# Performance work log

Measured on AMD Instinct MI355X. Metric: run time of the kernel, lower is better.

The kernel has to match this reference:

```python
import jax, jax.numpy as jnp
import numpy as np

B, N, C = 2, 20000, 256
TEST_MAX_BOX = 5000
IOU_THRESHOLDS = (0.4, 0.6, 0.8)
N_HIDDEN_LAYERS = 6  # six Conv1d(256,256,k=1)+LeakyReLU blocks in mask_w_layers


def setup_inputs() -> dict:
    key = jax.random.key(0)
    ks = jax.random.split(key, 8)
    # valid xyxy boxes: top-left in [0,900), w/h in [4,84)
    xy = jax.random.uniform(ks[0], (B, 2, N), dtype=jnp.float32) * 900.0
    wh = jax.random.uniform(ks[1], (B, 2, N), dtype=jnp.float32) * 80.0 + 4.0
    box = jnp.concatenate([xy, xy + wh], axis=1)              # [B,4,N]
    score = jax.random.uniform(ks[2], (B, 1, N), dtype=jnp.float32)
    feat = jax.random.normal(ks[3], (B, C, N), dtype=jnp.float32)
    W = jax.random.normal(ks[4], (N_HIDDEN_LAYERS, C, C), dtype=jnp.float32) * 0.02
    b = jnp.zeros((N_HIDDEN_LAYERS, C), dtype=jnp.float32)
    Wf = jax.random.normal(ks[5], (len(IOU_THRESHOLDS), C), dtype=jnp.float32) * 0.02
    bf = jnp.zeros((len(IOU_THRESHOLDS),), dtype=jnp.float32)
    return {"box": box, "score": score, "feat": feat, "W": W, "b": b, "Wf": Wf, "bf": bf}


def _box_iou(a, bxs):
    # a: [N,4], bxs: [M,4], xyxy -> [N,M] (torchvision ops.box_iou)
    area_a = (a[:, 2] - a[:, 0]) * (a[:, 3] - a[:, 1])
    area_b = (bxs[:, 2] - bxs[:, 0]) * (bxs[:, 3] - bxs[:, 1])
    lt = jnp.maximum(a[:, None, :2], bxs[None, :, :2])
    rb = jnp.minimum(a[:, None, 2:], bxs[None, :, 2:])
    wh = jnp.clip(rb - lt, 0.0)
    inter = wh[..., 0] * wh[..., 1]
    return inter / (area_a[:, None] + area_b[None, :] - inter)


def reference(box, score, feat, W, b, Wf, bf):
    # forward_test path of LMM
    boxT = jnp.swapaxes(box, 1, 2)                 # [B,N,4]
    s = jnp.swapaxes(score, 1, 2)[..., 0]          # [B,N]
    top_s, keep = jax.lax.top_k(s, TEST_MAX_BOX)   # [B,K] each, sorted desc
    boxK = jnp.take_along_axis(boxT, keep[..., None], axis=1)   # [B,K,4]
    featK = jnp.take_along_axis(feat, keep[:, None, :], axis=2)  # [B,C,K]

    iou = jax.vmap(_box_iou)(boxK, boxK)           # [B,K,K]
    idx = jnp.arange(TEST_MAX_BOX)
    masks = []
    for thr in IOU_THRESHOLDS:
        adjc = jnp.where(iou >= thr, 1.0, 0.0) * top_s[:, :, None]  # [B,K,K]
        max_idx = jnp.argmax(adjc, axis=1)                           # [B,K]
        masks.append((max_idx == idx[None, :]).astype(featK.dtype))
    masks = jnp.stack(masks, axis=1)               # [B,3,K]

    x = featK
    for l in range(N_HIDDEN_LAYERS):
        x = jax.nn.leaky_relu(jnp.einsum('oi,bik->bok', W[l], x) + b[l][:, None], 0.2)
    mask_w = jax.nn.softmax(jnp.einsum('oi,bik->bok', Wf, x) + bf[:, None], axis=1)  # [B,3,K]

    loc_max = jnp.sum(masks * mask_w, axis=1, keepdims=True)  # [B,1,K]
    return (loc_max, keep)
```

## Files before the change

### kernel.cpp

```cpp
#include <hip/hip_runtime.h>

#define B_  2
#define N_  20000
#define C_  256
#define K_  5000
#define M_  (B_ * K_)
#define CAP_ 5376
#define NBIN_ 2048
#define AST_ 264
#define RT_  21
#define RCH_ 7
#define RCT_ 3

typedef __attribute__((ext_vector_type(8))) short bf16x8;
typedef __attribute__((ext_vector_type(4))) float f32x4;
typedef __attribute__((ext_vector_type(2))) unsigned long long ull2;

__device__ __forceinline__ unsigned short f2bf(float x) {
  unsigned u = __float_as_uint(x);
  return (unsigned short)((u + 0x7fffu + ((u >> 16) & 1u)) >> 16);
}
__device__ __forceinline__ float bf2f(unsigned short h) {
  return __uint_as_float(((unsigned)h) << 16);
}
__device__ __forceinline__ unsigned fkey(float f) {
  unsigned u = __float_as_uint(f);
  return (u & 0x80000000u) ? ~u : (u | 0x80000000u);
}
__device__ __forceinline__ int binof(float s) {
  int b = (int)(s * 2048.0f);
  return b < 0 ? 0 : (b > 2047 ? 2047 : b);
}
__device__ __forceinline__ bf16x8 as_bf(uint4 v) {
  union { uint4 u; bf16x8 b; } c; c.u = v; return c.b;
}

__global__ __launch_bounds__(256) void k_prep(const float* __restrict__ W,
                                              unsigned short* __restrict__ Whi,
                                              int* __restrict__ nc,
                                              int* __restrict__ cnt2) {
  const int u = blockIdx.x;
  const int t = threadIdx.x;
  if (u >= 192) {
    if (u == 234) { if (t < B_) nc[t] = 0; return; }
    const int i = (u - 192) * 256 + t;
    if (i < B_ * CAP_) cnt2[i] = 0;
    return;
  }
  const int idx = u * 256 + t;
  const int lane = idx & 63;
  const int oi = (idx >> 6) & 1;
  const int ks = (idx >> 7) & 7;
  const int w = (idx >> 10) & 7;
  const int l = idx >> 13;
  const int o = w * 32 + oi * 16 + (lane & 15);
  const int k0 = ks * 32 + (lane >> 4) * 8;
  const float* src = W + ((size_t)(l * C_ + o)) * C_ + k0;
  float4 w0 = *(const float4*)&src[0];
  float4 w1 = *(const float4*)&src[4];
  const float wv[8] = {w0.x, w0.y, w0.z, w0.w, w1.x, w1.y, w1.z, w1.w};
  unsigned short hs[8];
#pragma unroll
  for (int q = 0; q < 8; ++q) hs[q] = f2bf(wv[q]);
  *(uint4*)&Whi[(size_t)idx * 8] = *(const uint4*)&hs[0];
}

__global__ __launch_bounds__(256) void k_selcomp(const float* __restrict__ score,
                                                 int* __restrict__ nc,
                                                 unsigned long long* __restrict__ ck,
                                                 int* __restrict__ rnk) {
  const int b = blockIdx.y;
  const float* s = score + b * N_;
  __shared__ int h[NBIN_];
  __shared__ int chs[256];
  __shared__ int res[1];
  const int t = threadIdx.x;
  for (int i = t; i < NBIN_; i += 256) h[i] = 0;
  __syncthreads();
  for (int i = t; i < N_; i += 256) atomicAdd(&h[binof(s[i])], 1);
  __syncthreads();
  int sum = 0;
#pragma unroll
  for (int j = 0; j < 8; ++j) sum += h[t * 8 + j];
  chs[t] = sum;
  __syncthreads();
  for (int off = 1; off < 256; off <<= 1) {
    int v = chs[t] + ((t + off < 256) ? chs[t + off] : 0);
    __syncthreads();
    chs[t] = v;
    __syncthreads();
  }
  const int above = (t + 1 < 256) ? chs[t + 1] : 0;
  if (above < K_ && K_ <= chs[t]) {
    int acc = above;
    for (int i = 7; i >= 0; --i) {
      const int bin = t * 8 + i;
      if (acc + h[bin] >= K_) { res[0] = bin; break; }
      acc += h[bin];
    }
  }
  __syncthreads();
  const int selB = res[0];
  const int n = blockIdx.x * 256 + t;
  if (n < N_) {
    rnk[b * N_ + n] = K_;
    const float sv = s[n];
    if (binof(sv) >= selB) {
      const int pos = atomicAdd(&nc[b], 1);
      if (pos < CAP_)
        ck[b * CAP_ + pos] =
            ((unsigned long long)fkey(sv) << 32) | (unsigned)(N_ - 1 - n);
    }
  }
}

__global__ __launch_bounds__(256) void k_rank2(const int* __restrict__ nc,
                                               const unsigned long long* __restrict__ ck,
                                               int* __restrict__ cnt2) {
  const int b = blockIdx.z;
  int S = nc[b]; if (S > CAP_) S = CAP_;
  __shared__ unsigned long long sk[256];
  const int t = threadIdx.x;
  const int j = blockIdx.x * 256 + t;
  const unsigned long long* kb = ck + b * CAP_;
  const unsigned long long myk = (j < S) ? kb[j] : 0ULL;
  int c = 0;
  const int nt = (S + 255) >> 8;
  int t0 = blockIdx.y * RCT_, t1 = t0 + RCT_;
  if (t1 > nt) t1 = nt;
  for (int tt = t0; tt < t1; ++tt) {
    const int gi = tt * 256 + t;
    unsigned long long kk = (gi < S) ? kb[gi] : 0ULL;
    __syncthreads();
    sk[t] = kk;
    __syncthreads();
#pragma unroll 8
    for (int ii = 0; ii < 256; ii += 2) {
      ull2 v = *(const ull2*)&sk[ii];
      c += (int)(v.x > myk) + (int)(v.y > myk);
    }
  }
  if (j < S && c > 0) atomicAdd(&cnt2[b * CAP_ + j], c);
}

__global__ __launch_bounds__(256) void k_scatter2(const int* __restrict__ nc,
                                                  const unsigned long long* __restrict__ ck,
                                                  const int* __restrict__ cnt2,
                                                  const float* __restrict__ box,
                                                  int* __restrict__ keep_i,
                                                  float* __restrict__ out_keep,
                                                  int* __restrict__ rnk,
                                                  float* __restrict__ boxK,
                                                  unsigned* __restrict__ maxiou) {
  const int b = blockIdx.y;
  int S = nc[b]; if (S > CAP_) S = CAP_;
  const int j = blockIdx.x * 256 + threadIdx.x;
  if (j >= S) return;
  const int c = cnt2[b * CAP_ + j];
  if (c >= K_) return;
  const int n = N_ - 1 - (int)(ck[b * CAP_ + j] & 0xffffffffu);
  keep_i[b * K_ + c] = n;
  out_keep[b * K_ + c] = (float)n;
  rnk[b * N_ + n] = c;
  const float* bb = box + (size_t)b * 4 * N_;
  float4 v;
  v.x = bb[n]; v.y = bb[N_ + n]; v.z = bb[2 * N_ + n]; v.w = bb[3 * N_ + n];
  ((float4*)boxK)[b * K_ + c] = v;
  maxiou[b * K_ + c] = 0u;
}

__global__ __launch_bounds__(256) void k_ioug(const float* __restrict__ boxK,
                                              unsigned* __restrict__ maxiou,
                                              const int* __restrict__ rnk,
                                              const float* __restrict__ feat,
                                              unsigned short* __restrict__ Xhi) {
  __shared__ __align__(16) char arena[16640];
  const int u = blockIdx.x;
  const int t = threadIdx.x;
  if (u < 420) {
    const int b = u / 210;
    const int p = u % 210;
    int jt = 0;
    while ((jt + 1) * (jt + 2) / 2 <= p) ++jt;
    const int it = p - jt * (jt + 1) / 2;
    float* sx0 = (float*)arena;
    float* sy0 = sx0 + 256; float* sx1 = sy0 + 256;
    float* sy1 = sx1 + 256; float* sa = sy1 + 256;
    const int gi0 = it * 256;
    const int gl = gi0 + t;
    if (gl < K_) {
      float4 v = ((const float4*)boxK)[b * K_ + gl];
      sx0[t] = v.x; sy0[t] = v.y; sx1[t] = v.z; sy1[t] = v.w;
      sa[t] = __fmul_rn(__fsub_rn(v.z, v.x), __fsub_rn(v.w, v.y));
    } else {
      sx0[t] = 1e30f; sy0[t] = 1e30f; sx1[t] = -1e30f; sy1[t] = -1e30f;
      sa[t] = 0.f;
    }
    __syncthreads();
    const int j = jt * 256 + t;
    if (j >= K_) return;
    float4 v = ((const float4*)boxK)[b * K_ + j];
    const float aj = __fmul_rn(__fsub_rn(v.z, v.x), __fsub_rn(v.w, v.y));
    float mx = 0.f;
    int lim = j - gi0;
    if (lim > 256) lim = 256;
    for (int ii = 0; ii < lim; ++ii) {
      float ltx = fmaxf(sx0[ii], v.x);
      float lty = fmaxf(sy0[ii], v.y);
      float rbx = fminf(sx1[ii], v.z);
      float rby = fminf(sy1[ii], v.w);
      float wx = fmaxf(__fsub_rn(rbx, ltx), 0.f);
      float wy = fmaxf(__fsub_rn(rby, lty), 0.f);
      float inter = __fmul_rn(wx, wy);
      if (inter > 0.f) {
        float uni = __fsub_rn(__fadd_rn(sa[ii], aj), inter);
        mx = fmaxf(mx, __fdiv_rn(inter, uni));
      }
    }
    if (mx > 0.f) atomicMax(&maxiou[b * K_ + j], __float_as_uint(mx));
  } else {
    const int v2 = u - 420;
    const int b = v2 / 1252;
    const int rem = v2 % 1252;
    const int c0 = (rem / 313) * 64;
    const int n0 = (rem % 313) * 64;
    float* T = (float*)arena;
    const int nl = t & 63, wq = t >> 6;
#pragma unroll
    for (int r = 0; r < 16; ++r) {
      const int cl = r * 4 + wq;
      const int n = n0 + nl;
      T[nl * 65 + cl] =
          (n < N_) ? feat[((size_t)(b * C_ + c0 + cl)) * N_ + n] : 0.f;
    }
    __syncthreads();
    const int nn = n0 + (t >> 2);
    if (nn >= N_) return;
    const int r = rnk[b * N_ + nn];
    if (r >= K_) return;
    const int cseg = (t & 3) * 16;
    unsigned short hb[16];
#pragma unroll
    for (int i = 0; i < 16; ++i)
      hb[i] = f2bf(T[(t >> 2) * 65 + cseg + i]);
    const size_t base = (size_t)(b * K_ + r) * C_ + c0 + cseg;
    *(uint4*)&Xhi[base] = *(const uint4*)&hb[0];
    *(uint4*)&Xhi[base + 8] = *(const uint4*)&hb[8];
  }
}

__global__ __launch_bounds__(512, 2) void k_mlp6(
    const unsigned short* __restrict__ Whi,
    const float* __restrict__ bias, const float* __restrict__ Wf,
    const float* __restrict__ bf, const unsigned* __restrict__ maxiou,
    const unsigned short* __restrict__ Xhi,
    float* __restrict__ out_loc) {
  __shared__ unsigned short act_hi[32 * AST_];
  __shared__ float swf[768];
  const int t = threadIdx.x;
  const int m0 = blockIdx.x * 32;

  {
    const int r = t >> 4;
    const int cs = (t & 15) * 16;
    const size_t g = (size_t)(m0 + r) * C_ + cs;
    *(uint4*)&act_hi[r * AST_ + cs] = *(const uint4*)&Xhi[g];
    *(uint4*)&act_hi[r * AST_ + cs + 8] = *(const uint4*)&Xhi[g + 8];
  }
  for (int i = t; i < 768; i += 512) swf[i] = Wf[i];
  __syncthreads();

  const int lane = t & 63;
  const int w = t >> 6;
  const int quad = lane >> 4, l15 = lane & 15;

  for (int l = 0; l < 6; ++l) {
    const size_t wbase = (size_t)(l * 8 + w) * 8192 + (size_t)lane * 8;
    f32x4 acc[2][2];
#pragma unroll
    for (int mi = 0; mi < 2; ++mi)
#pragma unroll
      for (int oi = 0; oi < 2; ++oi) acc[mi][oi] = (f32x4)0.f;
    uint4 nwh[2];
#pragma unroll
    for (int oi = 0; oi < 2; ++oi)
      nwh[oi] = *(const uint4*)&Whi[wbase + oi * 512];
#pragma unroll
    for (int ks = 0; ks < 8; ++ks) {
      bf16x8 wh[2];
#pragma unroll
      for (int oi = 0; oi < 2; ++oi) wh[oi] = as_bf(nwh[oi]);
      if (ks < 7) {
        const size_t nb = wbase + (size_t)(ks + 1) * 1024;
#pragma unroll
        for (int oi = 0; oi < 2; ++oi)
          nwh[oi] = *(const uint4*)&Whi[nb + oi * 512];
      }
      bf16x8 Ah[2];
#pragma unroll
      for (int mi = 0; mi < 2; ++mi)
        Ah[mi] = *(const bf16x8*)&act_hi[(mi * 16 + l15) * AST_ + ks * 32 + quad * 8];
#pragma unroll
      for (int mi = 0; mi < 2; ++mi)
#pragma unroll
        for (int oi = 0; oi < 2; ++oi)
          acc[mi][oi] = __builtin_amdgcn_mfma_f32_16x16x32_bf16(Ah[mi], wh[oi], acc[mi][oi], 0, 0, 0);
    }
    __syncthreads();
#pragma unroll
    for (int oi = 0; oi < 2; ++oi) {
      const int col = w * 32 + oi * 16 + l15;
      const float bb = bias[l * C_ + col];
#pragma unroll
      for (int mi = 0; mi < 2; ++mi)
#pragma unroll
        for (int r = 0; r < 4; ++r) {
          float y = acc[mi][oi][r] + bb;
          y = fmaxf(y, 0.2f * y);
          act_hi[(mi * 16 + quad * 4 + r) * AST_ + col] = f2bf(y);
        }
    }
    __syncthreads();
  }

  const int r = t >> 4;
  const int part = t & 15;
  const int m = m0 + r;
  float a0 = 0.f, a1 = 0.f, a2 = 0.f;
  for (int c = part * 16; c < part * 16 + 16; c += 2) {
    const unsigned hv = *(const unsigned*)&act_hi[r * AST_ + c];
    const float x0 = __uint_as_float((hv & 0xffffu) << 16);
    const float x1 = __uint_as_float(hv & 0xffff0000u);
    a0 += swf[c] * x0 + swf[c + 1] * x1;
    a1 += swf[256 + c] * x0 + swf[256 + c + 1] * x1;
    a2 += swf[512 + c] * x0 + swf[512 + c + 1] * x1;
  }
#pragma unroll
  for (int off = 1; off < 16; off <<= 1) {
    a0 += __shfl_xor(a0, off);
    a1 += __shfl_xor(a1, off);
    a2 += __shfl_xor(a2, off);
  }
  if (part == 0 && m < M_) {
    a0 += bf[0]; a1 += bf[1]; a2 += bf[2];
    const float mxv = fmaxf(a0, fmaxf(a1, a2));
    const float e0 = expf(a0 - mxv);
    const float e1 = expf(a1 - mxv);
    const float e2 = expf(a2 - mxv);
    const float inv = 1.f / (e0 + e1 + e2);
    const float miou = __uint_as_float(maxiou[m]);
    float loc = 0.f;
    if (miou < 0.4f) loc += e0;
    if (miou < 0.6f) loc += e1;
    if (miou < 0.8f) loc += e2;
    out_loc[m] = loc * inv;
  }
}

extern "C" void kernel_launch(void* const* d_in, const int* in_sizes, int n_in,
                              void* d_out, int out_size, void* d_ws, size_t ws_size,
                              hipStream_t stream) {
  const float* box   = (const float*)d_in[0];
  const float* score = (const float*)d_in[1];
  const float* feat  = (const float*)d_in[2];
  const float* W     = (const float*)d_in[3];
  const float* bias  = (const float*)d_in[4];
  const float* Wf    = (const float*)d_in[5];
  const float* bf    = (const float*)d_in[6];

  float* out = (float*)d_out;
  float* out_loc  = out;
  float* out_keep = out + M_;

  char* ws = (char*)d_ws;
  int*            keep_i = (int*)(ws + 0);
  float*          boxK   = (float*)(ws + 40960);
  unsigned*       maxiou = (unsigned*)(ws + 201216);
  unsigned short* Whi    = (unsigned short*)(ws + 241664);
  unsigned short* XtA_hi = (unsigned short*)(ws + 1814528);
  int*                rnk    = (int*)(ws + 12169216);
  unsigned long long* ck     = (unsigned long long*)(ws + 12329216);
  int*                cnt2   = (int*)(ws + 12415232);
  int*                nc     = (int*)(ws + 12458240);

  k_prep<<<235, 256, 0, stream>>>(W, Whi, nc, cnt2);
  k_selcomp<<<dim3(79, B_), 256, 0, stream>>>(score, nc, ck, rnk);
  k_rank2<<<dim3(RT_, RCH_, B_), 256, 0, stream>>>(nc, ck, cnt2);
  k_scatter2<<<dim3(RT_, B_), 256, 0, stream>>>(nc, ck, cnt2, box, keep_i,
                                                out_keep, rnk, boxK, maxiou);
  k_ioug<<<2924, 256, 0, stream>>>(boxK, maxiou, rnk, feat, XtA_hi);
  k_mlp6<<<313, 512, 0, stream>>>(Whi, bias, Wf, bf, maxiou, XtA_hi, out_loc);
}
```

Before: 196.0 us.

## Hoist score histogram into prep kernel, simplify rank loop, transpose MFMA epilogue

The per-batch histogram and threshold-bin search move out of k_selcomp, which had every one of its 158 blocks redo the full 20000-element histogram, into two extra blocks of k_prep that write the threshold bin to a workspace slot. k_rank2 drops its LDS staging and barriers and instead reads candidate keys straight from global memory with a uniform loop bounded by the valid count. k_mlp6 swaps the MFMA operand order so each lane holds four consecutive output channels, which allows a float4 bias load and packed 8-byte bf16 stores to LDS. The rank change trades shared-memory broadcast for global/L1 scalar loads, which could be slower.

Measured after the change: 213.4 us. 8.9% more time.

```diff
diff --git a/kernel.cpp b/kernel.cpp
--- a/kernel.cpp
+++ b/kernel.cpp
@@ -14,15 +14,11 @@
 
 typedef __attribute__((ext_vector_type(8))) short bf16x8;
 typedef __attribute__((ext_vector_type(4))) float f32x4;
-typedef __attribute__((ext_vector_type(2))) unsigned long long ull2;
 
 __device__ __forceinline__ unsigned short f2bf(float x) {
   unsigned u = __float_as_uint(x);
   return (unsigned short)((u + 0x7fffu + ((u >> 16) & 1u)) >> 16);
 }
-__device__ __forceinline__ float bf2f(unsigned short h) {
-  return __uint_as_float(((unsigned)h) << 16);
-}
 __device__ __forceinline__ unsigned fkey(float f) {
   unsigned u = __float_as_uint(f);
   return (u & 0x80000000u) ? ~u : (u | 0x80000000u);
@@ -36,13 +32,46 @@
 }
 
 __global__ __launch_bounds__(256) void k_prep(const float* __restrict__ W,
+                                              const float* __restrict__ score,
                                               unsigned short* __restrict__ Whi,
                                               int* __restrict__ nc,
-                                              int* __restrict__ cnt2) {
+                                              int* __restrict__ cnt2,
+                                              int* __restrict__ selb) {
   const int u = blockIdx.x;
   const int t = threadIdx.x;
   if (u >= 192) {
     if (u == 234) { if (t < B_) nc[t] = 0; return; }
+    if (u >= 235) {
+      const int b = u - 235;
+      __shared__ int h[NBIN_];
+      __shared__ int chs[256];
+      const float* s = score + b * N_;
+      for (int i = t; i < NBIN_; i += 256) h[i] = 0;
+      __syncthreads();
+      for (int i = t; i < N_; i += 256) atomicAdd(&h[binof(s[i])], 1);
+      __syncthreads();
+      int sum = 0;
+#pragma unroll
+      for (int j = 0; j < 8; ++j) sum += h[t * 8 + j];
+      chs[t] = sum;
+      __syncthreads();
+      for (int off = 1; off < 256; off <<= 1) {
+        int v = chs[t] + ((t + off < 256) ? chs[t + off] : 0);
+        __syncthreads();
+        chs[t] = v;
+        __syncthreads();
+      }
+      const int above = (t + 1 < 256) ? chs[t + 1] : 0;
+      if (above < K_ && K_ <= chs[t]) {
+        int acc = above;
+        for (int i = 7; i >= 0; --i) {
+          const int bin = t * 8 + i;
+          if (acc + h[bin] >= K_) { selb[b] = bin; break; }
+          acc += h[bin];
+        }
+      }
+      return;
+    }
     const int i = (u - 192) * 256 + t;
     if (i < B_ * CAP_) cnt2[i] = 0;
     return;
@@ -66,42 +95,14 @@
 }
 
 __global__ __launch_bounds__(256) void k_selcomp(const float* __restrict__ score,
+                                                 const int* __restrict__ selb,
                                                  int* __restrict__ nc,
                                                  unsigned long long* __restrict__ ck,
                                                  int* __restrict__ rnk) {
   const int b = blockIdx.y;
   const float* s = score + b * N_;
-  __shared__ int h[NBIN_];
-  __shared__ int chs[256];
-  __shared__ int res[1];
-  const int t = threadIdx.x;
-  for (int i = t; i < NBIN_; i += 256) h[i] = 0;
-  __syncthreads();
-  for (int i = t; i < N_; i += 256) atomicAdd(&h[binof(s[i])], 1);
-  __syncthreads();
-  int sum = 0;
-#pragma unroll
-  for (int j = 0; j < 8; ++j) sum += h[t * 8 + j];
-  chs[t] = sum;
-  __syncthreads();
-  for (int off = 1; off < 256; off <<= 1) {
-    int v = chs[t] + ((t + off < 256) ? chs[t + off] : 0);
-    __syncthreads();
-    chs[t] = v;
-    __syncthreads();
-  }
-  const int above = (t + 1 < 256) ? chs[t + 1] : 0;
-  if (above < K_ && K_ <= chs[t]) {
-    int acc = above;
-    for (int i = 7; i >= 0; --i) {
-      const int bin = t * 8 + i;
-      if (acc + h[bin] >= K_) { res[0] = bin; break; }
-      acc += h[bin];
-    }
-  }
-  __syncthreads();
-  const int selB = res[0];
-  const int n = blockIdx.x * 256 + t;
+  const int selB = selb[b];
+  const int n = blockIdx.x * 256 + threadIdx.x;
   if (n < N_) {
     rnk[b * N_ + n] = K_;
     const float sv = s[n];
@@ -119,7 +120,6 @@
                                                int* __restrict__ cnt2) {
   const int b = blockIdx.z;
   int S = nc[b]; if (S > CAP_) S = CAP_;
-  __shared__ unsigned long long sk[256];
   const int t = threadIdx.x;
   const int j = blockIdx.x * 256 + t;
   const unsigned long long* kb = ck + b * CAP_;
@@ -129,16 +129,13 @@
   int t0 = blockIdx.y * RCT_, t1 = t0 + RCT_;
   if (t1 > nt) t1 = nt;
   for (int tt = t0; tt < t1; ++tt) {
-    const int gi = tt * 256 + t;
-    unsigned long long kk = (gi < S) ? kb[gi] : 0ULL;
-    __syncthreads();
-    sk[t] = kk;
-    __syncthreads();
+    const unsigned long long* tp = kb + tt * 256;
+    int lim = S - tt * 256;
+    if (lim > 256) lim = 256;
+    int cc = 0;
 #pragma unroll 8
-    for (int ii = 0; ii < 256; ii += 2) {
-      ull2 v = *(const ull2*)&sk[ii];
-      c += (int)(v.x > myk) + (int)(v.y > myk);
-    }
+    for (int ii = 0; ii < lim; ++ii) cc += (int)(tp[ii] > myk);
+    c += cc;
   }
   if (j < S && c > 0) atomicAdd(&cnt2[b * CAP_ + j], c);
 }
@@ -255,7 +252,7 @@
     const float* __restrict__ bf, const unsigned* __restrict__ maxiou,
     const unsigned short* __restrict__ Xhi,
     float* __restrict__ out_loc) {
-  __shared__ unsigned short act_hi[32 * AST_];
+  __shared__ __align__(16) unsigned short act_hi[32 * AST_];
   __shared__ float swf[768];
   const int t = threadIdx.x;
   const int m0 = blockIdx.x * 32;
@@ -278,9 +275,9 @@
     const size_t wbase = (size_t)(l * 8 + w) * 8192 + (size_t)lane * 8;
     f32x4 acc[2][2];
 #pragma unroll
-    for (int mi = 0; mi < 2; ++mi)
-#pragma unroll
-      for (int oi = 0; oi < 2; ++oi) acc[mi][oi] = (f32x4)0.f;
+    for (int oi = 0; oi < 2; ++oi)
+#pragma unroll
+      for (int mi = 0; mi < 2; ++mi) acc[oi][mi] = (f32x4)0.f;
     uint4 nwh[2];
 #pragma unroll
     for (int oi = 0; oi < 2; ++oi)
@@ -304,21 +301,24 @@
       for (int mi = 0; mi < 2; ++mi)
 #pragma unroll
         for (int oi = 0; oi < 2; ++oi)
-          acc[mi][oi] = __builtin_amdgcn_mfma_f32_16x16x32_bf16(Ah[mi], wh[oi], acc[mi][oi], 0, 0, 0);
+          acc[oi][mi] = __builtin_amdgcn_mfma_f32_16x16x32_bf16(wh[oi], Ah[mi], acc[oi][mi], 0, 0, 0);
     }
     __syncthreads();
+    const int o0 = w * 32 + quad * 4;
 #pragma unroll
     for (int oi = 0; oi < 2; ++oi) {
-      const int col = w * 32 + oi * 16 + l15;
-      const float bb = bias[l * C_ + col];
-#pragma unroll
-      for (int mi = 0; mi < 2; ++mi)
-#pragma unroll
-        for (int r = 0; r < 4; ++r) {
-          float y = acc[mi][oi][r] + bb;
-          y = fmaxf(y, 0.2f * y);
-          act_hi[(mi * 16 + quad * 4 + r) * AST_ + col] = f2bf(y);
-        }
+      const float4 bb = *(const float4*)&bias[l * C_ + o0 + oi * 16];
+#pragma unroll
+      for (int mi = 0; mi < 2; ++mi) {
+        float y0 = acc[oi][mi][0] + bb.x; y0 = fmaxf(y0, 0.2f * y0);
+        float y1 = acc[oi][mi][1] + bb.y; y1 = fmaxf(y1, 0.2f * y1);
+        float y2 = acc[oi][mi][2] + bb.z; y2 = fmaxf(y2, 0.2f * y2);
+        float y3 = acc[oi][mi][3] + bb.w; y3 = fmaxf(y3, 0.2f * y3);
+        uint2 pk;
+        pk.x = (unsigned)f2bf(y0) | ((unsigned)f2bf(y1) << 16);
+        pk.y = (unsigned)f2bf(y2) | ((unsigned)f2bf(y3) << 16);
+        *(uint2*)&act_hi[(mi * 16 + l15) * AST_ + o0 + oi * 16] = pk;
+      }
     }
     __syncthreads();
   }
@@ -382,9 +382,10 @@
   unsigned long long* ck     = (unsigned long long*)(ws + 12329216);
   int*                cnt2   = (int*)(ws + 12415232);
   int*                nc     = (int*)(ws + 12458240);
-
-  k_prep<<<235, 256, 0, stream>>>(W, Whi, nc, cnt2);
-  k_selcomp<<<dim3(79, B_), 256, 0, stream>>>(score, nc, ck, rnk);
+  int*                selb   = (int*)(ws + 12458248);
+
+  k_prep<<<237, 256, 0, stream>>>(W, score, Whi, nc, cnt2, selb);
+  k_selcomp<<<dim3(79, B_), 256, 0, stream>>>(score, selb, nc, ck, rnk);
   k_rank2<<<dim3(RT_, RCH_, B_), 256, 0, stream>>>(nc, ck, cnt2);
   k_scatter2<<<dim3(RT_, B_), 256, 0, stream>>>(nc, ck, cnt2, box, keep_i,
                                                 out_keep, rnk, boxK, maxiou);
```
